# Optimization experiments

Hardware: AMD Instinct MI355X
Metric: run time of the kernel (lower is better)

Reference implementation:

```python
import jax, jax.numpy as jnp
import numpy as np

B, N, F_IN, D = 4, 2048, 32, 64  # D = output_dim; gat1: heads=4, d=D//2=32; gat2: heads=1, d=D


def _gat(x, adj_norm, Wq, bq, Wk, bk, Wv, bv, heads, d):
    b, n, _ = x.shape
    q = (x @ Wq + bq).reshape(b, n, heads, d)
    k = (x @ Wk + bk).reshape(b, n, heads, d)
    v = (x @ Wv + bv).reshape(b, n, heads, d)
    scores = jnp.einsum('bihd,bjhd->bhij', q, k) / jnp.sqrt(jnp.float32(d))
    mask = jnp.where(adj_norm == 0, jnp.float32(-1e9), jnp.float32(0.0))  # [N,N]
    w = jax.nn.softmax(scores + mask[None, None], axis=-1)
    out = jnp.einsum('bhij,bjhd->bihd', w, v)
    return out.reshape(b, n, heads * d)


def setup_inputs() -> dict:
    key = jax.random.key(0)
    ks = jax.random.split(key, 12)
    s = 0.05
    x = jax.random.normal(ks[0], (B, N, F_IN), dtype=jnp.float32)
    adj = (jax.random.uniform(ks[1], (N, N)) < 0.02).astype(jnp.float32)  # sparse binary graph
    return {
        'x': x, 'adj': adj,
        'Wp': jax.random.normal(ks[2], (F_IN, D)) * s, 'bp': jnp.zeros((D,), jnp.float32),
        'Wq1': jax.random.normal(ks[3], (F_IN, 2 * D)) * s, 'bq1': jnp.zeros((2 * D,), jnp.float32),
        'Wk1': jax.random.normal(ks[4], (F_IN, 2 * D)) * s, 'bk1': jnp.zeros((2 * D,), jnp.float32),
        'Wv1': jax.random.normal(ks[5], (F_IN, 2 * D)) * s, 'bv1': jnp.zeros((2 * D,), jnp.float32),
        'Wq2': jax.random.normal(ks[6], (2 * D, D)) * s, 'bq2': jnp.zeros((D,), jnp.float32),
        'Wk2': jax.random.normal(ks[7], (2 * D, D)) * s, 'bk2': jnp.zeros((D,), jnp.float32),
        'Wv2': jax.random.normal(ks[8], (2 * D, D)) * s, 'bv2': jnp.zeros((D,), jnp.float32),
        'gamma': jnp.ones((D,), jnp.float32), 'beta': jnp.zeros((D,), jnp.float32),
    }


def reference(x, adj, Wp, bp, Wq1, bq1, Wk1, bk1, Wv1, bv1,
              Wq2, bq2, Wk2, bk2, Wv2, bv2, gamma, beta):
    # row-normalized adjacency (normalize_adjacency)
    adj_n = adj / (jnp.sum(adj, axis=1, keepdims=True) + 1e-6)
    proj = x @ Wp + bp                                   # [B,N,D]
    h = _gat(x, adj_n, Wq1, bq1, Wk1, bk1, Wv1, bv1, 4, D // 2)   # [B,N,2D]
    h = jax.nn.relu(h)                                   # dropout inactive (training=False)
    h = _gat(h, adj_n, Wq2, bq2, Wk2, bk2, Wv2, bv2, 1, D)        # [B,N,D]
    y = h + proj
    mu = jnp.mean(y, axis=-1, keepdims=True)
    var = jnp.var(y, axis=-1, keepdims=True)
    return gamma * (y - mu) / jnp.sqrt(var + 1e-6) + beta
```

## Files before the change

kernel.cpp:

```cpp
#include <hip/hip_runtime.h>
#include <hip/hip_bf16.h>
#include <hip/hip_fp16.h>

#define BB 4
#define NN 2048
#define FIN 32
#define DD 64
#define MAXDEG 256

__device__ __forceinline__ __half2 u2h2(unsigned u) {
    union { unsigned u; __half2 h; } x; x.u = u; return x.h;
}

__global__ __launch_bounds__(128) void csr_gemm1(const float* __restrict__ adj,
    int* __restrict__ deg, int* __restrict__ col,
    const float* __restrict__ x,
    const float* __restrict__ Wp, const float* __restrict__ bp,
    const float* __restrict__ Wq, const float* __restrict__ bq,
    const float* __restrict__ Wk, const float* __restrict__ bk,
    const float* __restrict__ Wv, const float* __restrict__ bv,
    float* __restrict__ proj, __half* __restrict__ q1,
    __half* __restrict__ k1, __half* __restrict__ v1) {
    const int bid = blockIdx.x;
    const int tid = threadIdx.x;

    if (bid < NN / 2) {
        const int lane = tid & 63;
        const int i = bid * 2 + (tid >> 6);
        const unsigned long long below = (1ull << lane) - 1ull;
        int base = 0;
        for (int j0 = 0; j0 < NN; j0 += 256) {
            const float4 a = *(const float4*)(adj + (size_t)i * NN + j0 + lane * 4);
            const bool n0 = a.x != 0.0f, n1 = a.y != 0.0f, n2 = a.z != 0.0f, n3 = a.w != 0.0f;
            const unsigned long long m0 = __ballot(n0);
            const unsigned long long m1 = __ballot(n1);
            const unsigned long long m2 = __ballot(n2);
            const unsigned long long m3 = __ballot(n3);
            int slot = base + __popcll(m0 & below) + __popcll(m1 & below)
                            + __popcll(m2 & below) + __popcll(m3 & below);
            const int jb = j0 + 4 * lane;
            if (n0) { if (slot < MAXDEG) col[i * MAXDEG + slot] = jb;     ++slot; }
            if (n1) { if (slot < MAXDEG) col[i * MAXDEG + slot] = jb + 1; ++slot; }
            if (n2) { if (slot < MAXDEG) col[i * MAXDEG + slot] = jb + 2; ++slot; }
            if (n3) { if (slot < MAXDEG) col[i * MAXDEG + slot] = jb + 3; ++slot; }
            base += __popcll(m0) + __popcll(m1) + __popcll(m2) + __popcll(m3);
        }
        if (lane == 0) deg[i] = base < MAXDEG ? base : MAXDEG;
        return;
    }

    const int r0 = (bid - NN / 2) * 4;
    __shared__ float xs[FIN * 4];
    {
        const int r = tid >> 5, k = tid & 31;
        xs[k * 4 + r] = x[(size_t)r0 * FIN + tid];
    }
    __syncthreads();

    float aq0 = bq[tid], aq1 = aq0, aq2 = aq0, aq3 = aq0;
    float ak0 = bk[tid], ak1 = ak0, ak2 = ak0, ak3 = ak0;
    float av0 = bv[tid], av1 = av0, av2 = av0, av3 = av0;
    #pragma unroll
    for (int k = 0; k < FIN; ++k) {
        const float wq = Wq[k * 128 + tid];
        const float wk = Wk[k * 128 + tid];
        const float wv = Wv[k * 128 + tid];
        const float4 xv = *(const float4*)&xs[k * 4];
        aq0 = fmaf(xv.x, wq, aq0); aq1 = fmaf(xv.y, wq, aq1);
        aq2 = fmaf(xv.z, wq, aq2); aq3 = fmaf(xv.w, wq, aq3);
        ak0 = fmaf(xv.x, wk, ak0); ak1 = fmaf(xv.y, wk, ak1);
        ak2 = fmaf(xv.z, wk, ak2); ak3 = fmaf(xv.w, wk, ak3);
        av0 = fmaf(xv.x, wv, av0); av1 = fmaf(xv.y, wv, av1);
        av2 = fmaf(xv.z, wv, av2); av3 = fmaf(xv.w, wv, av3);
    }
    q1[(size_t)(r0 + 0) * 128 + tid] = __float2half_rn(aq0);
    q1[(size_t)(r0 + 1) * 128 + tid] = __float2half_rn(aq1);
    q1[(size_t)(r0 + 2) * 128 + tid] = __float2half_rn(aq2);
    q1[(size_t)(r0 + 3) * 128 + tid] = __float2half_rn(aq3);
    k1[(size_t)(r0 + 0) * 128 + tid] = __float2half_rn(ak0);
    k1[(size_t)(r0 + 1) * 128 + tid] = __float2half_rn(ak1);
    k1[(size_t)(r0 + 2) * 128 + tid] = __float2half_rn(ak2);
    k1[(size_t)(r0 + 3) * 128 + tid] = __float2half_rn(ak3);
    v1[(size_t)(r0 + 0) * 128 + tid] = __float2half_rn(av0);
    v1[(size_t)(r0 + 1) * 128 + tid] = __float2half_rn(av1);
    v1[(size_t)(r0 + 2) * 128 + tid] = __float2half_rn(av2);
    v1[(size_t)(r0 + 3) * 128 + tid] = __float2half_rn(av3);

    if (tid < 64) {
        float a0 = bp[tid], a1 = a0, a2 = a0, a3 = a0;
        #pragma unroll
        for (int k = 0; k < FIN; ++k) {
            const float wp = Wp[k * 64 + tid];
            const float4 xv = *(const float4*)&xs[k * 4];
            a0 = fmaf(xv.x, wp, a0); a1 = fmaf(xv.y, wp, a1);
            a2 = fmaf(xv.z, wp, a2); a3 = fmaf(xv.w, wp, a3);
        }
        proj[(size_t)(r0 + 0) * 64 + tid] = a0; proj[(size_t)(r0 + 1) * 64 + tid] = a1;
        proj[(size_t)(r0 + 2) * 64 + tid] = a2; proj[(size_t)(r0 + 3) * 64 + tid] = a3;
    }
}

__global__ __launch_bounds__(192) void gemm2_fused(const __half* __restrict__ h,
    const float* __restrict__ Wq, const float* __restrict__ bq,
    const float* __restrict__ Wk, const float* __restrict__ bk,
    const float* __restrict__ Wv, const float* __restrict__ bv,
    __half* __restrict__ q2, __half* __restrict__ k2, __half* __restrict__ v2) {
    const int r0 = blockIdx.x * 8;
    const int tid = threadIdx.x;
    const int mat = tid / 64;
    const int c = tid & 63;
    __shared__ float xs[128][8];
    for (int idx = tid; idx < 512; idx += 192) {
        const __half2 hv = ((const __half2*)(h + (size_t)r0 * 128))[idx];
        const int flat = idx * 2;
        const int r = flat >> 7, k = flat & 127;
        xs[k][r] = __low2float(hv); xs[k + 1][r] = __high2float(hv);
    }
    __syncthreads();

    const float* __restrict__ W   = mat == 0 ? Wq : (mat == 1 ? Wk : Wv);
    const float* __restrict__ bia = mat == 0 ? bq : (mat == 1 ? bk : bv);
    __half* __restrict__ Y        = mat == 0 ? q2 : (mat == 1 ? k2 : v2);

    float acc[8];
    const float b0 = bia[c];
    #pragma unroll
    for (int r = 0; r < 8; ++r) acc[r] = b0;
    #pragma unroll 4
    for (int k = 0; k < 128; ++k) {
        const float w = W[(size_t)k * 64 + c];
        const float4 xa = *(const float4*)&xs[k][0];
        const float4 xb = *(const float4*)&xs[k][4];
        acc[0] = fmaf(xa.x, w, acc[0]); acc[1] = fmaf(xa.y, w, acc[1]);
        acc[2] = fmaf(xa.z, w, acc[2]); acc[3] = fmaf(xa.w, w, acc[3]);
        acc[4] = fmaf(xb.x, w, acc[4]); acc[5] = fmaf(xb.y, w, acc[5]);
        acc[6] = fmaf(xb.z, w, acc[6]); acc[7] = fmaf(xb.w, w, acc[7]);
    }
    #pragma unroll
    for (int r = 0; r < 8; ++r) Y[(size_t)(r0 + r) * 64 + c] = __float2half_rn(acc[r]);
}

__device__ __forceinline__ void map_bi(int bid, int& b, int& i) {
    const int xcd = bid & 7;
    const int w = bid >> 3;
    b = xcd & 3;
    i = ((xcd >> 2) << 10) | w;
}

__global__ __launch_bounds__(128) void attn1_relu(const __half* __restrict__ q1,
                                                  const __half* __restrict__ k1,
                                                  const __half* __restrict__ v1,
                                                  const int* __restrict__ deg,
                                                  const int* __restrict__ col,
                                                  __half* __restrict__ h) {
    int b, i;
    map_bi(blockIdx.x, b, i);
    const int tid = threadIdx.x;

    __shared__ int nbr[MAXDEG];
    __shared__ __half2 qs2[64];
    __shared__ float wsA[4 * MAXDEG];
    __shared__ float2 part[2][64];
    __shared__ int sdeg;

    const size_t stride = (size_t)NN * 128;
    if (tid == 0) sdeg = deg[i];
    if (tid < 64) qs2[tid] = ((const __half2*)(q1 + (size_t)b * stride + (size_t)i * 128))[tid];
    __syncthreads();
    const int d = sdeg;
    for (int s = tid; s < d; s += 128) nbr[s] = col[i * MAXDEG + s];
    __syncthreads();

    const float scale = 0.17677669529663687f;
    const int hh = tid >> 5;
    const int t  = tid & 31;
    const int nr = (d + 31) >> 5;

    __half2 qh2[16];
    #pragma unroll
    for (int w = 0; w < 16; ++w) qh2[w] = qs2[hh * 16 + w];

    float sc[8];
    for (int r = 0; r < nr; ++r) {
        const int idx = r * 32 + t;
        float s = -INFINITY;
        if (idx < d) {
            const int j = nbr[idx];
            const uint4* kr4 = (const uint4*)(k1 + (size_t)b * stride + (size_t)j * 128 + hh * 32);
            __half2 a2 = __float2half2_rn(0.0f), b2 = __float2half2_rn(0.0f);
            #pragma unroll
            for (int w = 0; w < 4; ++w) {
                const uint4 kw = kr4[w];
                a2 = __hfma2(qh2[w * 4 + 0], u2h2(kw.x), a2);
                b2 = __hfma2(qh2[w * 4 + 1], u2h2(kw.y), b2);
                a2 = __hfma2(qh2[w * 4 + 2], u2h2(kw.z), a2);
                b2 = __hfma2(qh2[w * 4 + 3], u2h2(kw.w), b2);
            }
            s = ((__low2float(a2) + __high2float(a2)) +
                 (__low2float(b2) + __high2float(b2))) * scale;
        }
        sc[r] = s;
    }

    float mx = sc[0];
    for (int r = 1; r < nr; ++r) mx = fmaxf(mx, sc[r]);
    #pragma unroll
    for (int off = 16; off >= 1; off >>= 1) mx = fmaxf(mx, __shfl_xor(mx, off));
    float se = 0.0f;
    for (int r = 0; r < nr; ++r) {
        const float e = __expf(sc[r] - mx);
        sc[r] = e;
        se += e;
    }
    #pragma unroll
    for (int off = 16; off >= 1; off >>= 1) se += __shfl_xor(se, off);
    const float inv = (d > 0) ? 1.0f / se : 0.0f;
    for (int r = 0; r < nr; ++r) {
        const int idx = r * 32 + t;
        if (idx < d) wsA[hh * MAXDEG + idx] = sc[r] * inv;
    }
    __syncthreads();

    const int wv = tid >> 6;
    const int l  = tid & 63;
    const int hB = l >> 4;
    const __half* __restrict__ vrow = v1 + (size_t)b * stride + 2 * l;
    const float* __restrict__ wp = wsA + hB * MAXDEG;
    float a0 = 0.0f, a1 = 0.0f, b0 = 0.0f, b1 = 0.0f;
    int t2 = wv;
    for (; t2 + 2 < d; t2 += 4) {
        const int ja = nbr[t2], jb = nbr[t2 + 2];
        const __half2 va = u2h2(*(const unsigned*)(vrow + (size_t)ja * 128));
        const __half2 vb = u2h2(*(const unsigned*)(vrow + (size_t)jb * 128));
        const float wa = wp[t2], wb = wp[t2 + 2];
        a0 = fmaf(wa, __low2float(va), a0); a1 = fmaf(wa, __high2float(va), a1);
        b0 = fmaf(wb, __low2float(vb), b0); b1 = fmaf(wb, __high2float(vb), b1);
    }
    if (t2 < d) {
        const int ja = nbr[t2];
        const __half2 va = u2h2(*(const unsigned*)(vrow + (size_t)ja * 128));
        const float wa = wp[t2];
        a0 = fmaf(wa, __low2float(va), a0); a1 = fmaf(wa, __high2float(va), a1);
    }
    part[wv][l] = make_float2(a0 + b0, a1 + b1);
    __syncthreads();

    if (tid < 64) {
        float o0 = part[0][tid].x + part[1][tid].x;
        float o1 = part[0][tid].y + part[1][tid].y;
        if (d == 0) {
            float s0 = 0.0f, s1 = 0.0f;
            const __half* vr = v1 + (size_t)b * stride + 2 * tid;
            for (int j = 0; j < NN; ++j) {
                const __half2 vj = u2h2(*(const unsigned*)(vr + (size_t)j * 128));
                s0 += __low2float(vj); s1 += __high2float(vj);
            }
            o0 = s0 * (1.0f / NN); o1 = s1 * (1.0f / NN);
        }
        o0 = fmaxf(o0, 0.0f); o1 = fmaxf(o1, 0.0f);
        ((__half2*)(h + (size_t)b * stride + (size_t)i * 128))[tid] =
            __halves2half2(__float2half_rn(o0), __float2half_rn(o1));
    }
}

__global__ __launch_bounds__(64) void attn2_ln(const __half* __restrict__ q2,
                                               const __half* __restrict__ k2,
                                               const __half* __restrict__ v2,
                                               const float* __restrict__ proj,
                                               const int* __restrict__ deg,
                                               const int* __restrict__ col,
                                               const float* __restrict__ gamma,
                                               const float* __restrict__ beta,
                                               float* __restrict__ out) {
    int b, i;
    map_bi(blockIdx.x, b, i);
    const int lane = threadIdx.x;

    __shared__ int nbr[MAXDEG];
    __shared__ __half2 qs2[32];
    __shared__ float wsA[MAXDEG];
    __shared__ float att_lds[64];
    __shared__ int sdeg;

    const size_t stride = (size_t)NN * 64;
    if (lane == 0) sdeg = deg[i];
    if (lane < 32) qs2[lane] = ((const __half2*)(q2 + (size_t)b * stride + (size_t)i * 64))[lane];
    __syncthreads();
    const int d = sdeg;
    for (int s = lane; s < d; s += 64) nbr[s] = col[i * MAXDEG + s];
    __syncthreads();

    const float scale = 0.125f;
    const int nr = (d + 63) >> 6;

    __half2 qh2[32];
    #pragma unroll
    for (int w = 0; w < 32; ++w) qh2[w] = qs2[w];

    float sc[4];
    for (int r = 0; r < nr; ++r) {
        const int idx = r * 64 + lane;
        float s = -INFINITY;
        if (idx < d) {
            const int j = nbr[idx];
            const uint4* kr4 = (const uint4*)(k2 + (size_t)b * stride + (size_t)j * 64);
            __half2 a2 = __float2half2_rn(0.0f), b2 = __float2half2_rn(0.0f);
            #pragma unroll
            for (int w = 0; w < 8; ++w) {
                const uint4 kw = kr4[w];
                a2 = __hfma2(qh2[w * 4 + 0], u2h2(kw.x), a2);
                b2 = __hfma2(qh2[w * 4 + 1], u2h2(kw.y), b2);
                a2 = __hfma2(qh2[w * 4 + 2], u2h2(kw.z), a2);
                b2 = __hfma2(qh2[w * 4 + 3], u2h2(kw.w), b2);
            }
            s = ((__low2float(a2) + __high2float(a2)) +
                 (__low2float(b2) + __high2float(b2))) * scale;
        }
        sc[r] = s;
    }

    float mx = sc[0];
    for (int r = 1; r < nr; ++r) mx = fmaxf(mx, sc[r]);
    #pragma unroll
    for (int off = 32; off >= 1; off >>= 1) mx = fmaxf(mx, __shfl_xor(mx, off));
    float se = 0.0f;
    for (int r = 0; r < nr; ++r) {
        const float e = __expf(sc[r] - mx);
        sc[r] = e;
        se += e;
    }
    #pragma unroll
    for (int off = 32; off >= 1; off >>= 1) se += __shfl_xor(se, off);
    const float inv = (d > 0) ? 1.0f / se : 0.0f;
    for (int r = 0; r < nr; ++r) {
        const int idx = r * 64 + lane;
        if (idx < d) wsA[idx] = sc[r] * inv;
    }
    __syncthreads();

    const int p = lane & 31, g = lane >> 5;
    const __half* __restrict__ vrow = v2 + (size_t)b * stride + 2 * p;
    float a0 = 0.0f, a1 = 0.0f, b0 = 0.0f, b1 = 0.0f;
    int t2 = g;
    for (; t2 + 2 < d; t2 += 4) {
        const int ja = nbr[t2], jb = nbr[t2 + 2];
        const __half2 va = u2h2(*(const unsigned*)(vrow + (size_t)ja * 64));
        const __half2 vb = u2h2(*(const unsigned*)(vrow + (size_t)jb * 64));
        const float wa = wsA[t2], wb = wsA[t2 + 2];
        a0 = fmaf(wa, __low2float(va), a0); a1 = fmaf(wa, __high2float(va), a1);
        b0 = fmaf(wb, __low2float(vb), b0); b1 = fmaf(wb, __high2float(vb), b1);
    }
    if (t2 < d) {
        const int ja = nbr[t2];
        const __half2 va = u2h2(*(const unsigned*)(vrow + (size_t)ja * 64));
        const float wa = wsA[t2];
        a0 = fmaf(wa, __low2float(va), a0); a1 = fmaf(wa, __high2float(va), a1);
    }
    a0 += b0; a1 += b1;
    a0 += __shfl_xor(a0, 32);
    a1 += __shfl_xor(a1, 32);
    if (g == 0) { att_lds[2 * p] = a0; att_lds[2 * p + 1] = a1; }
    __syncthreads();
    float att = att_lds[lane];
    if (d == 0) {
        float a = 0.0f;
        const __half* vr = v2 + (size_t)b * stride + lane;
        for (int j = 0; j < NN; ++j) a += __half2float(vr[(size_t)j * 64]);
        att = a * (1.0f / NN);
    }

    const float y = att + proj[(size_t)b * stride + (size_t)i * 64 + lane];
    float s = y;
    s += __shfl_xor(s, 32); s += __shfl_xor(s, 16); s += __shfl_xor(s, 8);
    s += __shfl_xor(s, 4);  s += __shfl_xor(s, 2);  s += __shfl_xor(s, 1);
    const float mu = s * (1.0f / 64.0f);
    const float yc = y - mu;
    float sq = yc * yc;
    sq += __shfl_xor(sq, 32); sq += __shfl_xor(sq, 16); sq += __shfl_xor(sq, 8);
    sq += __shfl_xor(sq, 4);  sq += __shfl_xor(sq, 2);  sq += __shfl_xor(sq, 1);
    const float var = sq * (1.0f / 64.0f);
    out[(size_t)b * stride + (size_t)i * 64 + lane] =
        gamma[lane] * yc * rsqrtf(var + 1e-6f) + beta[lane];
}

extern "C" void kernel_launch(void* const* d_in, const int* in_sizes, int n_in,
                              void* d_out, int out_size, void* d_ws, size_t ws_size,
                              hipStream_t stream) {
    const float* x     = (const float*)d_in[0];
    const float* adj   = (const float*)d_in[1];
    const float* Wp    = (const float*)d_in[2];
    const float* bp    = (const float*)d_in[3];
    const float* Wq1   = (const float*)d_in[4];
    const float* bq1   = (const float*)d_in[5];
    const float* Wk1   = (const float*)d_in[6];
    const float* bk1   = (const float*)d_in[7];
    const float* Wv1   = (const float*)d_in[8];
    const float* bv1   = (const float*)d_in[9];
    const float* Wq2   = (const float*)d_in[10];
    const float* bq2   = (const float*)d_in[11];
    const float* Wk2   = (const float*)d_in[12];
    const float* bk2   = (const float*)d_in[13];
    const float* Wv2   = (const float*)d_in[14];
    const float* bv2   = (const float*)d_in[15];
    const float* gamma = (const float*)d_in[16];
    const float* beta  = (const float*)d_in[17];
    float* out = (float*)d_out;

    char* ws = (char*)d_ws;
    size_t off = 0;
    auto alloc = [&](size_t bytes) {
        void* p = ws + off;
        off = (off + bytes + 255) & ~(size_t)255;
        return p;
    };
    int*    deg  = (int*)   alloc((size_t)NN * 4);
    int*    col  = (int*)   alloc((size_t)NN * MAXDEG * 4);
    float*  proj = (float*) alloc((size_t)BB * NN * 64 * 4);
    __half* q1   = (__half*)alloc((size_t)BB * NN * 128 * 2);
    __half* k1   = (__half*)alloc((size_t)BB * NN * 128 * 2);
    __half* v1   = (__half*)alloc((size_t)BB * NN * 128 * 2);
    __half* h    = (__half*)alloc((size_t)BB * NN * 128 * 2);
    __half* q2   = (__half*)alloc((size_t)BB * NN * 64 * 2);
    __half* k2   = (__half*)alloc((size_t)BB * NN * 64 * 2);
    __half* v2   = (__half*)alloc((size_t)BB * NN * 64 * 2);

    csr_gemm1<<<NN / 2 + BB * NN / 4, 128, 0, stream>>>(
        adj, deg, col, x, Wp, bp, Wq1, bq1, Wk1, bk1, Wv1, bv1, proj, q1, k1, v1);

    attn1_relu<<<BB * NN, 128, 0, stream>>>(q1, k1, v1, deg, col, h);

    gemm2_fused<<<BB * NN / 8, 192, 0, stream>>>(h, Wq2, bq2, Wk2, bk2, Wv2, bv2,
                                                 q2, k2, v2);

    attn2_ln<<<BB * NN, 64, 0, stream>>>(q2, k2, v2, proj, deg, col, gamma, beta, out);
}
```

Baseline: 66.23 us.

## Map one wavefront per attention row and drop block barriers and LDS staging

Both attention kernels now pack four rows per 256-thread block, with each 64-lane wavefront handling one (batch,row) pair. Block-wide __syncthreads and shared-memory staging of neighbour indices and q are replaced by direct global loads and per-wave LDS buffers fenced with s_waitcnt. MAXDEG drops from 256 to 128, shrinking the CSR buffer and LDS, and the value aggregation in attn1 is unrolled by four using int4 column loads. This relies on a single wave owning its LDS slice and on no row having more than 128 neighbours, which holds for the test graph's ~2% density but is a tighter assumption than before.

```diff
diff --git a/kernel.cpp b/kernel.cpp
--- a/kernel.cpp
+++ b/kernel.cpp
@@ -6,7 +6,7 @@
 #define NN 2048
 #define FIN 32
 #define DD 64
-#define MAXDEG 256
+#define MAXDEG 128
 
 __device__ __forceinline__ __half2 u2h2(unsigned u) {
     union { unsigned u; __half2 h; } x; x.u = u; return x.h;
@@ -140,52 +140,47 @@
     for (int r = 0; r < 8; ++r) Y[(size_t)(r0 + r) * 64 + c] = __float2half_rn(acc[r]);
 }
 
-__device__ __forceinline__ void map_bi(int bid, int& b, int& i) {
+__device__ __forceinline__ void map_bi4(int bid, int wid, int& b, int& i) {
     const int xcd = bid & 7;
-    const int w = bid >> 3;
     b = xcd & 3;
-    i = ((xcd >> 2) << 10) | w;
-}
-
-__global__ __launch_bounds__(128) void attn1_relu(const __half* __restrict__ q1,
+    i = ((xcd >> 2) << 10) | ((bid >> 3) << 2) | wid;
+}
+
+__global__ __launch_bounds__(256) void attn1_relu(const __half* __restrict__ q1,
                                                   const __half* __restrict__ k1,
                                                   const __half* __restrict__ v1,
                                                   const int* __restrict__ deg,
                                                   const int* __restrict__ col,
                                                   __half* __restrict__ h) {
+    const int wid = threadIdx.x >> 6;
+    const int lane = threadIdx.x & 63;
     int b, i;
-    map_bi(blockIdx.x, b, i);
-    const int tid = threadIdx.x;
-
-    __shared__ int nbr[MAXDEG];
-    __shared__ __half2 qs2[64];
-    __shared__ float wsA[4 * MAXDEG];
-    __shared__ float2 part[2][64];
-    __shared__ int sdeg;
-
+    map_bi4(blockIdx.x, wid, b, i);
+
+    __shared__ float wsA[4][4][MAXDEG + 8];
     const size_t stride = (size_t)NN * 128;
-    if (tid == 0) sdeg = deg[i];
-    if (tid < 64) qs2[tid] = ((const __half2*)(q1 + (size_t)b * stride + (size_t)i * 128))[tid];
-    __syncthreads();
-    const int d = sdeg;
-    for (int s = tid; s < d; s += 128) nbr[s] = col[i * MAXDEG + s];
-    __syncthreads();
+    const int d = deg[i];
+    const int hh = lane >> 4;
+    const int t  = lane & 15;
+
+    const uint4* qp4 = (const uint4*)(q1 + (size_t)b * stride + (size_t)i * 128 + hh * 32);
+    __half2 qh2[16];
+    {
+        const uint4 qa = qp4[0], qb = qp4[1], qc = qp4[2], qd = qp4[3];
+        qh2[0]  = u2h2(qa.x); qh2[1]  = u2h2(qa.y); qh2[2]  = u2h2(qa.z); qh2[3]  = u2h2(qa.w);
+        qh2[4]  = u2h2(qb.x); qh2[5]  = u2h2(qb.y); qh2[6]  = u2h2(qb.z); qh2[7]  = u2h2(qb.w);
+        qh2[8]  = u2h2(qc.x); qh2[9]  = u2h2(qc.y); qh2[10] = u2h2(qc.z); qh2[11] = u2h2(qc.w);
+        qh2[12] = u2h2(qd.x); qh2[13] = u2h2(qd.y); qh2[14] = u2h2(qd.z); qh2[15] = u2h2(qd.w);
+    }
 
     const float scale = 0.17677669529663687f;
-    const int hh = tid >> 5;
-    const int t  = tid & 31;
-    const int nr = (d + 31) >> 5;
-
-    __half2 qh2[16];
-    #pragma unroll
-    for (int w = 0; w < 16; ++w) qh2[w] = qs2[hh * 16 + w];
-
+    const int nr = (d + 15) >> 4;
     float sc[8];
     for (int r = 0; r < nr; ++r) {
-        const int idx = r * 32 + t;
+        const int idx = r * 16 + t;
         float s = -INFINITY;
         if (idx < d) {
-            const int j = nbr[idx];
+            const int j = col[i * MAXDEG + idx];
             const uint4* kr4 = (const uint4*)(k1 + (size_t)b * stride + (size_t)j * 128 + hh * 32);
             __half2 a2 = __float2half2_rn(0.0f), b2 = __float2half2_rn(0.0f);
             #pragma unroll
@@ -205,7 +200,7 @@
     float mx = sc[0];
     for (int r = 1; r < nr; ++r) mx = fmaxf(mx, sc[r]);
     #pragma unroll
-    for (int off = 16; off >= 1; off >>= 1) mx = fmaxf(mx, __shfl_xor(mx, off));
+    for (int off = 8; off >= 1; off >>= 1) mx = fmaxf(mx, __shfl_xor(mx, off));
     float se = 0.0f;
     for (int r = 0; r < nr; ++r) {
         const float e = __expf(sc[r] - mx);
@@ -213,96 +208,91 @@
         se += e;
     }
     #pragma unroll
-    for (int off = 16; off >= 1; off >>= 1) se += __shfl_xor(se, off);
+    for (int off = 8; off >= 1; off >>= 1) se += __shfl_xor(se, off);
     const float inv = (d > 0) ? 1.0f / se : 0.0f;
     for (int r = 0; r < nr; ++r) {
-        const int idx = r * 32 + t;
-        if (idx < d) wsA[hh * MAXDEG + idx] = sc[r] * inv;
-    }
-    __syncthreads();
-
-    const int wv = tid >> 6;
-    const int l  = tid & 63;
-    const int hB = l >> 4;
-    const __half* __restrict__ vrow = v1 + (size_t)b * stride + 2 * l;
-    const float* __restrict__ wp = wsA + hB * MAXDEG;
+        const int idx = r * 16 + t;
+        if (idx < d) wsA[wid][hh][idx] = sc[r] * inv;
+    }
+    asm volatile("s_waitcnt lgkmcnt(0)" ::: "memory");
+
+    const float* __restrict__ wp = wsA[wid][lane >> 4];
+    const int4* __restrict__ cp4 = (const int4*)(col + i * MAXDEG);
+    const __half* __restrict__ vrow = v1 + (size_t)b * stride + 2 * lane;
     float a0 = 0.0f, a1 = 0.0f, b0 = 0.0f, b1 = 0.0f;
-    int t2 = wv;
-    for (; t2 + 2 < d; t2 += 4) {
-        const int ja = nbr[t2], jb = nbr[t2 + 2];
-        const __half2 va = u2h2(*(const unsigned*)(vrow + (size_t)ja * 128));
-        const __half2 vb = u2h2(*(const unsigned*)(vrow + (size_t)jb * 128));
-        const float wa = wp[t2], wb = wp[t2 + 2];
-        a0 = fmaf(wa, __low2float(va), a0); a1 = fmaf(wa, __high2float(va), a1);
-        b0 = fmaf(wb, __low2float(vb), b0); b1 = fmaf(wb, __high2float(vb), b1);
-    }
-    if (t2 < d) {
-        const int ja = nbr[t2];
-        const __half2 va = u2h2(*(const unsigned*)(vrow + (size_t)ja * 128));
-        const float wa = wp[t2];
-        a0 = fmaf(wa, __low2float(va), a0); a1 = fmaf(wa, __high2float(va), a1);
-    }
-    part[wv][l] = make_float2(a0 + b0, a1 + b1);
-    __syncthreads();
-
-    if (tid < 64) {
-        float o0 = part[0][tid].x + part[1][tid].x;
-        float o1 = part[0][tid].y + part[1][tid].y;
-        if (d == 0) {
-            float s0 = 0.0f, s1 = 0.0f;
-            const __half* vr = v1 + (size_t)b * stride + 2 * tid;
-            for (int j = 0; j < NN; ++j) {
-                const __half2 vj = u2h2(*(const unsigned*)(vr + (size_t)j * 128));
-                s0 += __low2float(vj); s1 += __high2float(vj);
-            }
-            o0 = s0 * (1.0f / NN); o1 = s1 * (1.0f / NN);
-        }
-        o0 = fmaxf(o0, 0.0f); o1 = fmaxf(o1, 0.0f);
-        ((__half2*)(h + (size_t)b * stride + (size_t)i * 128))[tid] =
-            __halves2half2(__float2half_rn(o0), __float2half_rn(o1));
-    }
-}
-
-__global__ __launch_bounds__(64) void attn2_ln(const __half* __restrict__ q2,
-                                               const __half* __restrict__ k2,
-                                               const __half* __restrict__ v2,
-                                               const float* __restrict__ proj,
-                                               const int* __restrict__ deg,
-                                               const int* __restrict__ col,
-                                               const float* __restrict__ gamma,
-                                               const float* __restrict__ beta,
-                                               float* __restrict__ out) {
+    float c0 = 0.0f, c1 = 0.0f, e0 = 0.0f, e1 = 0.0f;
+    int t2 = 0;
+    for (; t2 + 4 <= d; t2 += 4) {
+        const int4 j4 = cp4[t2 >> 2];
+        const float w0 = wp[t2], w1 = wp[t2 + 1], w2 = wp[t2 + 2], w3 = wp[t2 + 3];
+        const __half2 v0 = u2h2(*(const unsigned*)(vrow + (size_t)j4.x * 128));
+        const __half2 v1h = u2h2(*(const unsigned*)(vrow + (size_t)j4.y * 128));
+        const __half2 v2h = u2h2(*(const unsigned*)(vrow + (size_t)j4.z * 128));
+        const __half2 v3h = u2h2(*(const unsigned*)(vrow + (size_t)j4.w * 128));
+        a0 = fmaf(w0, __low2float(v0), a0);  a1 = fmaf(w0, __high2float(v0), a1);
+        b0 = fmaf(w1, __low2float(v1h), b0); b1 = fmaf(w1, __high2float(v1h), b1);
+        c0 = fmaf(w2, __low2float(v2h), c0); c1 = fmaf(w2, __high2float(v2h), c1);
+        e0 = fmaf(w3, __low2float(v3h), e0); e1 = fmaf(w3, __high2float(v3h), e1);
+    }
+    for (; t2 < d; ++t2) {
+        const int j = col[i * MAXDEG + t2];
+        const float w0 = wp[t2];
+        const __half2 v0 = u2h2(*(const unsigned*)(vrow + (size_t)j * 128));
+        a0 = fmaf(w0, __low2float(v0), a0);  a1 = fmaf(w0, __high2float(v0), a1);
+    }
+    float o0 = (a0 + b0) + (c0 + e0);
+    float o1 = (a1 + b1) + (c1 + e1);
+    if (d == 0) {
+        float s0 = 0.0f, s1 = 0.0f;
+        for (int j = 0; j < NN; ++j) {
+            const __half2 vj = u2h2(*(const unsigned*)(vrow + (size_t)j * 128));
+            s0 += __low2float(vj); s1 += __high2float(vj);
+        }
+        o0 = s0 * (1.0f / NN); o1 = s1 * (1.0f / NN);
+    }
+    o0 = fmaxf(o0, 0.0f); o1 = fmaxf(o1, 0.0f);
+    ((__half2*)(h + (size_t)b * stride + (size_t)i * 128))[lane] =
+        __halves2half2(__float2half_rn(o0), __float2half_rn(o1));
+}
+
+__global__ __launch_bounds__(256) void attn2_ln(const __half* __restrict__ q2,
+                                                const __half* __restrict__ k2,
+                                                const __half* __restrict__ v2,
+                                                const float* __restrict__ proj,
+                                                const int* __restrict__ deg,
+                                                const int* __restrict__ col,
+                                                const float* __restrict__ gamma,
+                                                const float* __restrict__ beta,
+                                                float* __restrict__ out) {
+    const int wid = threadIdx.x >> 6;
+    const int lane = threadIdx.x & 63;
     int b, i;
-    map_bi(blockIdx.x, b, i);
-    const int lane = threadIdx.x;
-
-    __shared__ int nbr[MAXDEG];
-    __shared__ __half2 qs2[32];
-    __shared__ float wsA[MAXDEG];
-    __shared__ float att_lds[64];
-    __shared__ int sdeg;
-
+    map_bi4(blockIdx.x, wid, b, i);
+
+    __shared__ float ws2[4][MAXDEG];
+    __shared__ float att_lds[4][64];
     const size_t stride = (size_t)NN * 64;
-    if (lane == 0) sdeg = deg[i];
-    if (lane < 32) qs2[lane] = ((const __half2*)(q2 + (size_t)b * stride + (size_t)i * 64))[lane];
-    __syncthreads();
-    const int d = sdeg;
-    for (int s = lane; s < d; s += 64) nbr[s] = col[i * MAXDEG + s];
-    __syncthreads();
+    const int d = deg[i];
+
+    __half2 qh2[32];
+    {
+        const uint4* qp4 = (const uint4*)(q2 + (size_t)b * stride + (size_t)i * 64);
+        #pragma unroll
+        for (int w = 0; w < 8; ++w) {
+            const uint4 qw = qp4[w];
+            qh2[w * 4 + 0] = u2h2(qw.x); qh2[w * 4 + 1] = u2h2(qw.y);
+            qh2[w * 4 + 2] = u2h2(qw.z); qh2[w * 4 + 3] = u2h2(qw.w);
+        }
+    }
 
     const float scale = 0.125f;
     const int nr = (d + 63) >> 6;
-
-    __half2 qh2[32];
-    #pragma unroll
-    for (int w = 0; w < 32; ++w) qh2[w] = qs2[w];
-
-    float sc[4];
+    float sc[2];
     for (int r = 0; r < nr; ++r) {
         const int idx = r * 64 + lane;
         float s = -INFINITY;
         if (idx < d) {
-            const int j = nbr[idx];
+            const int j = col[i * MAXDEG + idx];
             const uint4* kr4 = (const uint4*)(k2 + (size_t)b * stride + (size_t)j * 64);
             __half2 a2 = __float2half2_rn(0.0f), b2 = __float2half2_rn(0.0f);
             #pragma unroll
@@ -334,34 +324,35 @@
     const float inv = (d > 0) ? 1.0f / se : 0.0f;
     for (int r = 0; r < nr; ++r) {
         const int idx = r * 64 + lane;
-        if (idx < d) wsA[idx] = sc[r] * inv;
-    }
-    __syncthreads();
+        if (idx < d) ws2[wid][idx] = sc[r] * inv;
+    }
+    asm volatile("s_waitcnt lgkmcnt(0)" ::: "memory");
 
     const int p = lane & 31, g = lane >> 5;
+    const float* __restrict__ wp = ws2[wid];
     const __half* __restrict__ vrow = v2 + (size_t)b * stride + 2 * p;
     float a0 = 0.0f, a1 = 0.0f, b0 = 0.0f, b1 = 0.0f;
     int t2 = g;
     for (; t2 + 2 < d; t2 += 4) {
-        const int ja = nbr[t2], jb = nbr[t2 + 2];
+        const int ja = col[i * MAXDEG + t2], jb = col[i * MAXDEG + t2 + 2];
         const __half2 va = u2h2(*(const unsigned*)(vrow + (size_t)ja * 64));
         const __half2 vb = u2h2(*(const unsigned*)(vrow + (size_t)jb * 64));
-        const float wa = wsA[t2], wb = wsA[t2 + 2];
+        const float wa = wp[t2], wb = wp[t2 + 2];
         a0 = fmaf(wa, __low2float(va), a0); a1 = fmaf(wa, __high2float(va), a1);
         b0 = fmaf(wb, __low2float(vb), b0); b1 = fmaf(wb, __high2float(vb), b1);
     }
     if (t2 < d) {
-        const int ja = nbr[t2];
+        const int ja = col[i * MAXDEG + t2];
         const __half2 va = u2h2(*(const unsigned*)(vrow + (size_t)ja * 64));
-        const float wa = wsA[t2];
+        const float wa = wp[t2];
         a0 = fmaf(wa, __low2float(va), a0); a1 = fmaf(wa, __high2float(va), a1);
     }
     a0 += b0; a1 += b1;
     a0 += __shfl_xor(a0, 32);
     a1 += __shfl_xor(a1, 32);
-    if (g == 0) { att_lds[2 * p] = a0; att_lds[2 * p + 1] = a1; }
-    __syncthreads();
-    float att = att_lds[lane];
+    if (g == 0) { att_lds[wid][2 * p] = a0; att_lds[wid][2 * p + 1] = a1; }
+    asm volatile("s_waitcnt lgkmcnt(0)" ::: "memory");
+    float att = att_lds[wid][lane];
     if (d == 0) {
         float a = 0.0f;
         const __half* vr = v2 + (size_t)b * stride + lane;
@@ -427,10 +418,10 @@
     csr_gemm1<<<NN / 2 + BB * NN / 4, 128, 0, stream>>>(
         adj, deg, col, x, Wp, bp, Wq1, bq1, Wk1, bk1, Wv1, bv1, proj, q1, k1, v1);
 
-    attn1_relu<<<BB * NN, 128, 0, stream>>>(q1, k1, v1, deg, col, h);
+    attn1_relu<<<BB * NN / 4, 256, 0, stream>>>(q1, k1, v1, deg, col, h);
 
     gemm2_fused<<<BB * NN / 8, 192, 0, stream>>>(h, Wq2, bq2, Wk2, bk2, Wv2, bv2,
                                                  q2, k2, v2);
 
-    attn2_ln<<<BB * NN, 64, 0, stream>>>(q2, k2, v2, proj, deg, col, gamma, beta, out);
-}
+    attn2_ln<<<BB * NN / 4, 256, 0, stream>>>(q2, k2, v2, proj, deg, col, gamma, beta, out);
+}
```

Measured after the change: 66.81 us. About the same (+0.9%).
